# Optimization experiments

Hardware: AMD Instinct MI355X
Metric: run time of the kernel (lower is better)

The kernel has to match this reference:

```python
import jax, jax.numpy as jnp
import numpy as np

NDIM = 1024
NHEAD = 16
HEAD_DIM = NDIM // NHEAD


def setup_inputs() -> dict:
    key = jax.random.key(0)
    ks = jax.random.split(key, 12)
    B, L, C = 2, 2048, NDIM
    s = 0.02
    return {
        "q": jax.random.normal(ks[0], (B, L, C), jnp.float32),
        "k": jax.random.normal(ks[1], (B, L, C), jnp.float32),
        "v": jax.random.normal(ks[2], (B, L, C), jnp.float32),
        "Wq": jax.random.normal(ks[3], (C, C), jnp.float32) * s,
        "bq": jax.random.normal(ks[4], (C,), jnp.float32) * s,
        "Wk": jax.random.normal(ks[5], (C, C), jnp.float32) * s,
        "bk": jax.random.normal(ks[6], (C,), jnp.float32) * s,
        "Wv": jax.random.normal(ks[7], (C, C), jnp.float32) * s,
        "bv": jax.random.normal(ks[8], (C,), jnp.float32) * s,
        "Wo": jax.random.normal(ks[9], (C, C), jnp.float32) * s,
        "bo": jax.random.normal(ks[10], (C,), jnp.float32) * s,
    }


def reference(q, k, v, Wq, bq, Wk, bk, Wv, bv, Wo, bo):
    B, Lq, C = q.shape
    H, D = NHEAD, HEAD_DIM
    # projections, then split heads: (B, H, L, D)
    qh = (q @ Wq + bq).reshape(B, Lq, H, D).transpose(0, 2, 1, 3)
    kh = (k @ Wk + bk).reshape(B, k.shape[1], H, D).transpose(0, 2, 1, 3)
    vh = (v @ Wv + bv).reshape(B, v.shape[1], H, D).transpose(0, 2, 1, 3)
    scale = 1.0 / jnp.sqrt(jnp.asarray(D, qh.dtype))
    att = jnp.einsum("bhqd,bhkd->bhqk", qh, kh) * scale  # (B,H,Lq,Lk)
    att = jax.nn.softmax(att, axis=-1)  # dropout p=0.0 -> identity
    y = jnp.einsum("bhqk,bhkd->bhqd", att, vh)
    y = y.transpose(0, 2, 1, 3).reshape(B, Lq, C)
    return y @ Wo + bo
```

## Files before the change

kernel.cpp:

```cpp
#include <hip/hip_runtime.h>
#include <math.h>

#define BATCH 2
#define SEQ   2048
#define CDIM  1024
#define NHEAD 16
#define HDIM  64
#define TOKS  (BATCH * SEQ)

typedef __bf16 bf16x8 __attribute__((ext_vector_type(8)));
typedef __bf16 bf16x2 __attribute__((ext_vector_type(2)));
typedef float  f32x4  __attribute__((ext_vector_type(4)));
typedef float  f32x16 __attribute__((ext_vector_type(16)));

#define MFMA16(a, b, c) __builtin_amdgcn_mfma_f32_16x16x32_bf16(a, b, c, 0, 0, 0)
#define MFMA32(a, b, c) __builtin_amdgcn_mfma_f32_32x32x16_bf16(a, b, c, 0, 0, 0)

#define QSCALE 0.1803368801111204f

__device__ __forceinline__ void gload_lds16(const __bf16* g, __bf16* l) {
    __builtin_amdgcn_global_load_lds(
        (const __attribute__((address_space(1))) unsigned int*)g,
        (__attribute__((address_space(3))) unsigned int*)l, 16, 0, 0);
}

__global__ __launch_bounds__(256) void prep_kernel(
    const float* __restrict__ q, const float* __restrict__ k, const float* __restrict__ v,
    __bf16* __restrict__ qo, __bf16* __restrict__ ko, __bf16* __restrict__ vo,
    const float* __restrict__ W0, const float* __restrict__ W1,
    const float* __restrict__ W2, const float* __restrict__ W3,
    __bf16* __restrict__ T0, __bf16* __restrict__ T1,
    __bf16* __restrict__ T2, __bf16* __restrict__ T3)
{
    __shared__ __bf16 Ts[64][72];
    const int bx = blockIdx.x;
    const int tid = threadIdx.x;

    if (bx < 6144) {
        const int t = bx >> 11;
        const size_t i = ((size_t)(bx & 2047) * 256 + tid) * 8;
        const float* s = t == 0 ? q : (t == 1 ? k : v);
        __bf16* d = t == 0 ? qo : (t == 1 ? ko : vo);
        const float4 x = *(const float4*)&s[i];
        const float4 y = *(const float4*)&s[i + 4];
        bf16x8 o;
        o[0] = (__bf16)x.x; o[1] = (__bf16)x.y; o[2] = (__bf16)x.z; o[3] = (__bf16)x.w;
        o[4] = (__bf16)y.x; o[5] = (__bf16)y.y; o[6] = (__bf16)y.z; o[7] = (__bf16)y.w;
        *(bf16x8*)&d[i] = o;
        return;
    }

    const int t  = bx - 6144;
    const int z  = t >> 8;
    const int ry = (t & 255) >> 4;
    const int rx = t & 15;
    const float* W = z == 0 ? W0 : z == 1 ? W1 : z == 2 ? W2 : W3;
    __bf16* T = z == 0 ? T0 : z == 1 ? T1 : z == 2 ? T2 : T3;
    const int rb = ry * 64, cb = rx * 64;
    const int r = tid >> 4;
    const int c4 = (tid & 15) * 4;
#pragma unroll
    for (int p = 0; p < 4; p++) {
        const int rr = p * 16 + r;
        const float4 w4 = *(const float4*)&W[(size_t)(rb + rr) * CDIM + cb + c4];
        Ts[c4 + 0][rr] = (__bf16)w4.x;
        Ts[c4 + 1][rr] = (__bf16)w4.y;
        Ts[c4 + 2][rr] = (__bf16)w4.z;
        Ts[c4 + 3][rr] = (__bf16)w4.w;
    }
    __syncthreads();
    const int n = tid >> 2;
    const int k16 = (tid & 3) * 16;
    *(bf16x8*)&T[(size_t)(cb + n) * CDIM + rb + k16]     = *(const bf16x8*)&Ts[n][k16];
    *(bf16x8*)&T[(size_t)(cb + n) * CDIM + rb + k16 + 8] = *(const bf16x8*)&Ts[n][k16 + 8];
}

__global__ __launch_bounds__(512, 6) void qkv_gemm_kernel(
    const __bf16* __restrict__ qb, const __bf16* __restrict__ kb,
    const __bf16* __restrict__ vb,
    const __bf16* __restrict__ Wqt, const __bf16* __restrict__ Wkt,
    const __bf16* __restrict__ Wvt,
    const float* __restrict__ bq, const float* __restrict__ bk,
    const float* __restrict__ bv,
    __bf16* __restrict__ Qh, __bf16* __restrict__ Kh, __bf16* __restrict__ Vht)
{
    __shared__ __bf16 As[128 * 32];
    __shared__ __bf16 Bs[128 * 32];

    const int lin = blockIdx.x + (blockIdx.y << 3) + (blockIdx.z << 8);
    const int nl  = (lin & 7) * 96 + (lin >> 3);
    const int bx  = nl & 7;
    const int by  = (nl >> 3) & 31;
    const int z   = nl >> 8;

    const __bf16* A    = z == 0 ? qb : z == 1 ? kb : Wvt;
    const __bf16* Bt   = z == 0 ? Wqt : z == 1 ? Wkt : vb;
    const float*  bias = z == 0 ? bq : z == 1 ? bk : bv;

    const int tid  = threadIdx.x;
    const int w    = tid >> 6;
    const int lane = tid & 63;
    const int quad = lane >> 4;
    const int c    = lane & 15;
    const int wm   = w >> 1;
    const int wn   = w & 1;
    const int rowBase = (z == 2 ? bx : by) * 128;
    const int colBase = (z == 2 ? by : bx) * 128;

    const int sr = lane >> 2;
    const int sk = (lane & 3) * 8;

    f32x4 acc[2][4];
#pragma unroll
    for (int i = 0; i < 2; i++)
#pragma unroll
        for (int j = 0; j < 4; j++) acc[i][j] = (f32x4){0, 0, 0, 0};

    const __bf16* srcA = A  + (size_t)(rowBase + w * 16 + sr) * CDIM + sk;
    const __bf16* srcB = Bt + (size_t)(colBase + w * 16 + sr) * CDIM + sk;
    __bf16* dstA = &As[w * 16 * 32];
    __bf16* dstB = &Bs[w * 16 * 32];

    for (int k0 = 0; k0 < CDIM; k0 += 32) {
        gload_lds16(srcA + k0, dstA);
        gload_lds16(srcB + k0, dstB);
        __syncthreads();

        bf16x8 af[2], bf[4];
#pragma unroll
        for (int i = 0; i < 2; i++)
            af[i] = *(const bf16x8*)&As[(wm * 32 + i * 16 + c) * 32 + quad * 8];
#pragma unroll
        for (int i = 0; i < 4; i++)
            bf[i] = *(const bf16x8*)&Bs[(wn * 64 + i * 16 + c) * 32 + quad * 8];
#pragma unroll
        for (int mi = 0; mi < 2; mi++)
#pragma unroll
            for (int ni = 0; ni < 4; ni++)
                acc[mi][ni] = MFMA16(af[mi], bf[ni], acc[mi][ni]);
        __syncthreads();
    }

#pragma unroll
    for (int mi = 0; mi < 2; mi++) {
#pragma unroll
        for (int ni = 0; ni < 4; ni++) {
            const int col = colBase + wn * 64 + ni * 16 + c;
#pragma unroll
            for (int r = 0; r < 4; r++) {
                const int row = rowBase + wm * 32 + mi * 16 + quad * 4 + r;
                const float val = acc[mi][ni][r];
                if (z == 2) {
                    Vht[(size_t)row * TOKS + col] = (__bf16)(val + bias[row]);
                } else {
                    const int b = row >> 11, l = row & 2047;
                    const int h = col >> 6,  d = col & 63;
                    const float s = (z == 0) ? QSCALE : 1.0f;
                    __bf16* outp = (z == 0) ? Qh : Kh;
                    outp[((((size_t)b * NHEAD + h) * SEQ) + l) * HDIM + d] =
                        (__bf16)((val + bias[col]) * s);
                }
            }
        }
    }
}

__global__ __launch_bounds__(512, 4) void out_gemm_kernel(
    const __bf16* __restrict__ A, const __bf16* __restrict__ Bt,
    const float* __restrict__ bias, float* __restrict__ out)
{
    __shared__ __bf16 As[128 * 32];
    __shared__ __bf16 Bs[64 * 32];

    const int lin = blockIdx.x + (blockIdx.y << 4);
    const int nl  = (lin & 7) * 64 + (lin >> 3);
    const int bx  = nl & 15;
    const int by  = nl >> 4;

    const int tid  = threadIdx.x;
    const int w    = tid >> 6;
    const int lane = tid & 63;
    const int quad = lane >> 4;
    const int c    = lane & 15;
    const int wm   = w >> 1;
    const int wn   = w & 1;
    const int rowBase = by * 128;
    const int colBase = bx * 64;
    const int sr = lane >> 2;
    const int sk = (lane & 3) * 8;

    f32x4 acc[2][2];
#pragma unroll
    for (int i = 0; i < 2; i++)
#pragma unroll
        for (int j = 0; j < 2; j++) acc[i][j] = (f32x4){0, 0, 0, 0};

    const __bf16* srcA = A + (size_t)(rowBase + w * 16 + sr) * CDIM + sk;
    const __bf16* srcB = Bt + (size_t)(colBase + (w & 3) * 16 + sr) * CDIM + sk;
    __bf16* dstA = &As[w * 16 * 32];
    __bf16* dstB = &Bs[(w & 3) * 16 * 32];

    for (int k0 = 0; k0 < CDIM; k0 += 32) {
        gload_lds16(srcA + k0, dstA);
        if (w < 4) gload_lds16(srcB + k0, dstB);
        __syncthreads();

        bf16x8 af[2], bf[2];
#pragma unroll
        for (int i = 0; i < 2; i++)
            af[i] = *(const bf16x8*)&As[(wm * 32 + i * 16 + c) * 32 + quad * 8];
#pragma unroll
        for (int i = 0; i < 2; i++)
            bf[i] = *(const bf16x8*)&Bs[(wn * 32 + i * 16 + c) * 32 + quad * 8];
#pragma unroll
        for (int mi = 0; mi < 2; mi++)
#pragma unroll
            for (int ni = 0; ni < 2; ni++)
                acc[mi][ni] = MFMA16(af[mi], bf[ni], acc[mi][ni]);
        __syncthreads();
    }

#pragma unroll
    for (int mi = 0; mi < 2; mi++) {
#pragma unroll
        for (int ni = 0; ni < 2; ni++) {
            const int col = colBase + wn * 32 + ni * 16 + c;
#pragma unroll
            for (int r = 0; r < 4; r++) {
                const int row = rowBase + wm * 32 + mi * 16 + quad * 4 + r;
                out[(size_t)row * CDIM + col] = acc[mi][ni][r] + bias[col];
            }
        }
    }
}

__global__ __launch_bounds__(256, 2) void attn_v10_kernel(
    const __bf16* __restrict__ Qh, const __bf16* __restrict__ Kh,
    const __bf16* __restrict__ Vht, __bf16* __restrict__ Y)
{
    __shared__ __align__(16) __bf16 Ks[2][128][64];
    __shared__ __align__(16) __bf16 Vt[2][64][128];

    const int tid  = threadIdx.x;
    const int w    = tid >> 6;
    const int lane = tid & 63;
    const int l31  = lane & 31;
    const int hi   = lane >> 5;
    const int swz  = l31 & 7;
    const int bh   = blockIdx.x;
    const int b    = bh >> 4;
    const int h    = bh & 15;
    const int qbase = blockIdx.y * 128 + w * 32;

    const __bf16* Qg = Qh + (size_t)bh * SEQ * HDIM;
    const __bf16* Kg = Kh + (size_t)bh * SEQ * HDIM;
    const __bf16* Vg = Vht + (size_t)(h * HDIM) * TOKS + (size_t)b * SEQ;

    bf16x8 qf[4];
#pragma unroll
    for (int ks = 0; ks < 4; ks++)
        qf[ks] = *(const bf16x8*)&Qg[(size_t)(qbase + l31) * HDIM + ks * 16 + hi * 8];

    bf16x8 ones;
#pragma unroll
    for (int j = 0; j < 8; j++) ones[j] = (__bf16)1.0f;

    f32x16 O0, O1, LA;
#pragma unroll
    for (int j = 0; j < 16; j++) { O0[j] = 0.0f; O1[j] = 0.0f; LA[j] = 0.0f; }

    const int kr8 = lane >> 3, kc = lane & 7;
    const int vr4 = lane >> 4, vc = lane & 15;

#define STAGE(T, bb)                                                          \
    {                                                                         \
        _Pragma("unroll")                                                     \
        for (int jj = 0; jj < 4; jj++) {                                      \
            const int j = w * 4 + jj;                                         \
            gload_lds16(Kg + (size_t)((T) + 8 * j + kr8) * HDIM               \
                           + ((kc ^ kr8) * 8),                                \
                        &Ks[bb][8 * j][0]);                                   \
            gload_lds16(Vg + (size_t)(4 * j + vr4) * TOKS + (T)               \
                           + ((vc ^ ((4 * j + vr4) & 7)) * 8),                \
                        &Vt[bb][4 * j][0]);                                   \
        }                                                                     \
    }

    STAGE(0, 0);
    __syncthreads();

    int buf = 0;
    for (int t0 = 0; t0 < SEQ; t0 += 128) {
        const int tn = t0 + 128;
        if (tn < SEQ) {
            if (buf == 0) STAGE(tn, 1) else STAGE(tn, 0)
        }

#pragma unroll
        for (int kt = 0; kt < 4; kt++) {
            f32x16 st0, st1;
#pragma unroll
            for (int j = 0; j < 16; j++) { st0[j] = 0.0f; st1[j] = 0.0f; }
            const bf16x8 kf0 = *(const bf16x8*)&Ks[buf][kt * 32 + l31][((0 + hi) ^ swz) * 8];
            const bf16x8 kf1 = *(const bf16x8*)&Ks[buf][kt * 32 + l31][((2 + hi) ^ swz) * 8];
            const bf16x8 kf2 = *(const bf16x8*)&Ks[buf][kt * 32 + l31][((4 + hi) ^ swz) * 8];
            const bf16x8 kf3 = *(const bf16x8*)&Ks[buf][kt * 32 + l31][((6 + hi) ^ swz) * 8];
            st0 = MFMA32(kf0, qf[0], st0);
            st1 = MFMA32(kf1, qf[1], st1);
            st0 = MFMA32(kf2, qf[2], st0);
            st1 = MFMA32(kf3, qf[3], st1);

            float p[16];
#pragma unroll
            for (int j = 0; j < 16; j++)
                p[j] = __builtin_amdgcn_exp2f(st0[j] + st1[j]);

#pragma unroll
            for (int kl = 0; kl < 2; kl++) {
                const int r0 = kl * 8;
                union { bf16x2 v; unsigned int u; } pa, pb, pc, pd;
                pa.v[0] = (__bf16)p[r0 + 0]; pa.v[1] = (__bf16)p[r0 + 1];
                pb.v[0] = (__bf16)p[r0 + 2]; pb.v[1] = (__bf16)p[r0 + 3];
                pc.v[0] = (__bf16)p[r0 + 4]; pc.v[1] = (__bf16)p[r0 + 5];
                pd.v[0] = (__bf16)p[r0 + 6]; pd.v[1] = (__bf16)p[r0 + 7];
                asm volatile("v_permlane32_swap_b32 %0, %1"
                             : "+v"(pa.u), "+v"(pc.u));
                asm volatile("v_permlane32_swap_b32 %0, %1"
                             : "+v"(pb.u), "+v"(pd.u));
                union { unsigned int u[4]; bf16x8 v; } af;
                af.u[0] = pa.u; af.u[1] = pb.u; af.u[2] = pc.u; af.u[3] = pd.u;
                const int cc = kt * 4 + kl * 2 + hi;
                const bf16x8 vf0 = *(const bf16x8*)&Vt[buf][l31][(cc ^ swz) * 8];
                const bf16x8 vf1 = *(const bf16x8*)&Vt[buf][32 + l31][(cc ^ swz) * 8];
                __builtin_amdgcn_s_setprio(1);
                LA = MFMA32(af.v, ones, LA);
                O0 = MFMA32(af.v, vf0, O0);
                O1 = MFMA32(af.v, vf1, O1);
                __builtin_amdgcn_s_setprio(0);
            }
        }

        __syncthreads();
        buf ^= 1;
    }
#undef STAGE

    __bf16* Yb = Y + (size_t)b * SEQ * CDIM;
#pragma unroll
    for (int reg = 0; reg < 16; reg++) {
        const int qrow  = (reg & 3) + 8 * (reg >> 2) + 4 * hi;
        const float iq  = 1.0f / LA[reg];
        __bf16* yp = Yb + (size_t)(qbase + qrow) * CDIM + h * HDIM + l31;
        yp[0]  = (__bf16)(O0[reg] * iq);
        yp[32] = (__bf16)(O1[reg] * iq);
    }
}


extern "C" void kernel_launch(void* const* d_in, const int* in_sizes, int n_in,
                              void* d_out, int out_size, void* d_ws, size_t ws_size,
                              hipStream_t stream)
{
    const float* q  = (const float*)d_in[0];
    const float* k  = (const float*)d_in[1];
    const float* v  = (const float*)d_in[2];
    const float* Wq = (const float*)d_in[3];
    const float* bq = (const float*)d_in[4];
    const float* Wk = (const float*)d_in[5];
    const float* bk = (const float*)d_in[6];
    const float* Wv = (const float*)d_in[7];
    const float* bv = (const float*)d_in[8];
    const float* Wo = (const float*)d_in[9];
    const float* bo = (const float*)d_in[10];
    float* out = (float*)d_out;

    const size_t MAT = (size_t)TOKS * CDIM;
    const size_t WN  = (size_t)CDIM * CDIM;

    __bf16* p   = (__bf16*)d_ws;
    __bf16* qb  = p; p += MAT;
    __bf16* kb  = p; p += MAT;
    __bf16* vb  = p; p += MAT;
    __bf16* Wqt = p; p += WN;
    __bf16* Wkt = p; p += WN;
    __bf16* Wvt = p; p += WN;
    __bf16* Wot = p; p += WN;
    __bf16* Qh  = p; p += MAT;
    __bf16* Kh  = p; p += MAT;
    __bf16* Vht = p; p += MAT;
    __bf16* Yb  = qb;

    prep_kernel<<<dim3(7168), dim3(256), 0, stream>>>(
        q, k, v, qb, kb, vb, Wq, Wk, Wv, Wo, Wqt, Wkt, Wvt, Wot);

    qkv_gemm_kernel<<<dim3(8, 32, 3), dim3(512), 0, stream>>>(
        qb, kb, vb, Wqt, Wkt, Wvt, bq, bk, bv, Qh, Kh, Vht);

    attn_v10_kernel<<<dim3(BATCH * NHEAD, SEQ / 128), dim3(256), 0, stream>>>(Qh, Kh, Vht, Yb);

    out_gemm_kernel<<<dim3(16, 32), dim3(512), 0, stream>>>(Yb, Wot, bo, out);
}
```

Measured before the change: 218.7 us.

## Split attention key range across two wave groups and reduce partials via LDS

The attention kernel now launches 512 threads per block. The two halves of the waves each process half of the key sequence (1024 keys) for the same 128 query rows. Partial O and row-sum accumulators are combined through LDS scratch at the end. This doubles the waves per block and halves each wave's serial loop length, aiming for more latency hiding and occupancy. The cost is an extra reduction step and a barrier. There is no running max, so like the code before it relies on unnormalized exp2 staying in range.

```diff
diff --git a/kernel.cpp b/kernel.cpp
--- a/kernel.cpp
+++ b/kernel.cpp
@@ -234,15 +234,17 @@
     }
 }
 
-__global__ __launch_bounds__(256, 2) void attn_v10_kernel(
+__global__ __launch_bounds__(512, 4) void attn_v11_kernel(
     const __bf16* __restrict__ Qh, const __bf16* __restrict__ Kh,
     const __bf16* __restrict__ Vht, __bf16* __restrict__ Y)
 {
-    __shared__ __align__(16) __bf16 Ks[2][128][64];
-    __shared__ __align__(16) __bf16 Vt[2][64][128];
+    __shared__ __align__(16) __bf16 Ks[2][2][64][64];
+    __shared__ __align__(16) __bf16 Vt[2][2][64][64];
 
     const int tid  = threadIdx.x;
     const int w    = tid >> 6;
+    const int wq   = w & 3;
+    const int half = w >> 2;
     const int lane = tid & 63;
     const int l31  = lane & 31;
     const int hi   = lane >> 5;
@@ -250,7 +252,7 @@
     const int bh   = blockIdx.x;
     const int b    = bh >> 4;
     const int h    = bh & 15;
-    const int qbase = blockIdx.y * 128 + w * 32;
+    const int qbase = blockIdx.y * 128 + wq * 32;
 
     const __bf16* Qg = Qh + (size_t)bh * SEQ * HDIM;
     const __bf16* Kg = Kh + (size_t)bh * SEQ * HDIM;
@@ -270,19 +272,22 @@
     for (int j = 0; j < 16; j++) { O0[j] = 0.0f; O1[j] = 0.0f; LA[j] = 0.0f; }
 
     const int kr8 = lane >> 3, kc = lane & 7;
-    const int vr4 = lane >> 4, vc = lane & 15;
 
 #define STAGE(T, bb)                                                          \
     {                                                                         \
         _Pragma("unroll")                                                     \
         for (int jj = 0; jj < 4; jj++) {                                      \
-            const int j = w * 4 + jj;                                         \
-            gload_lds16(Kg + (size_t)((T) + 8 * j + kr8) * HDIM               \
-                           + ((kc ^ kr8) * 8),                                \
-                        &Ks[bb][8 * j][0]);                                   \
-            gload_lds16(Vg + (size_t)(4 * j + vr4) * TOKS + (T)               \
-                           + ((vc ^ ((4 * j + vr4) & 7)) * 8),                \
-                        &Vt[bb][4 * j][0]);                                   \
+            const int cch = w * 4 + jj;                                       \
+            const int s  = (cch >> 3) & 1;                                    \
+            const int j  = cch & 7;                                           \
+            if (cch < 16)                                                     \
+                gload_lds16(Kg + (size_t)(s * 1024 + (T) + 8 * j + kr8) * HDIM \
+                               + ((kc ^ kr8) * 8),                            \
+                            &Ks[bb][s][8 * j][0]);                            \
+            else                                                              \
+                gload_lds16(Vg + (size_t)(8 * j + kr8) * TOKS                 \
+                               + s * 1024 + (T) + ((kc ^ kr8) * 8),           \
+                            &Vt[bb][s][8 * j][0]);                            \
         }                                                                     \
     }
 
@@ -290,30 +295,30 @@
     __syncthreads();
 
     int buf = 0;
-    for (int t0 = 0; t0 < SEQ; t0 += 128) {
-        const int tn = t0 + 128;
-        if (tn < SEQ) {
+    for (int t0 = 0; t0 < 1024; t0 += 64) {
+        const int tn = t0 + 64;
+        if (tn < 1024) {
             if (buf == 0) STAGE(tn, 1) else STAGE(tn, 0)
         }
 
 #pragma unroll
-        for (int kt = 0; kt < 4; kt++) {
-            f32x16 st0, st1;
-#pragma unroll
-            for (int j = 0; j < 16; j++) { st0[j] = 0.0f; st1[j] = 0.0f; }
-            const bf16x8 kf0 = *(const bf16x8*)&Ks[buf][kt * 32 + l31][((0 + hi) ^ swz) * 8];
-            const bf16x8 kf1 = *(const bf16x8*)&Ks[buf][kt * 32 + l31][((2 + hi) ^ swz) * 8];
-            const bf16x8 kf2 = *(const bf16x8*)&Ks[buf][kt * 32 + l31][((4 + hi) ^ swz) * 8];
-            const bf16x8 kf3 = *(const bf16x8*)&Ks[buf][kt * 32 + l31][((6 + hi) ^ swz) * 8];
-            st0 = MFMA32(kf0, qf[0], st0);
-            st1 = MFMA32(kf1, qf[1], st1);
-            st0 = MFMA32(kf2, qf[2], st0);
-            st1 = MFMA32(kf3, qf[3], st1);
+        for (int kt = 0; kt < 2; kt++) {
+            f32x16 st;
+#pragma unroll
+            for (int j = 0; j < 16; j++) st[j] = 0.0f;
+            const bf16x8 kf0 = *(const bf16x8*)&Ks[buf][half][kt * 32 + l31][((0 + hi) ^ swz) * 8];
+            const bf16x8 kf1 = *(const bf16x8*)&Ks[buf][half][kt * 32 + l31][((2 + hi) ^ swz) * 8];
+            const bf16x8 kf2 = *(const bf16x8*)&Ks[buf][half][kt * 32 + l31][((4 + hi) ^ swz) * 8];
+            const bf16x8 kf3 = *(const bf16x8*)&Ks[buf][half][kt * 32 + l31][((6 + hi) ^ swz) * 8];
+            st = MFMA32(kf0, qf[0], st);
+            st = MFMA32(kf1, qf[1], st);
+            st = MFMA32(kf2, qf[2], st);
+            st = MFMA32(kf3, qf[3], st);
 
             float p[16];
 #pragma unroll
             for (int j = 0; j < 16; j++)
-                p[j] = __builtin_amdgcn_exp2f(st0[j] + st1[j]);
+                p[j] = __builtin_amdgcn_exp2f(st[j]);
 
 #pragma unroll
             for (int kl = 0; kl < 2; kl++) {
@@ -330,8 +335,8 @@
                 union { unsigned int u[4]; bf16x8 v; } af;
                 af.u[0] = pa.u; af.u[1] = pb.u; af.u[2] = pc.u; af.u[3] = pd.u;
                 const int cc = kt * 4 + kl * 2 + hi;
-                const bf16x8 vf0 = *(const bf16x8*)&Vt[buf][l31][(cc ^ swz) * 8];
-                const bf16x8 vf1 = *(const bf16x8*)&Vt[buf][32 + l31][(cc ^ swz) * 8];
+                const bf16x8 vf0 = *(const bf16x8*)&Vt[buf][half][l31][(cc ^ swz) * 8];
+                const bf16x8 vf1 = *(const bf16x8*)&Vt[buf][half][32 + l31][(cc ^ swz) * 8];
                 __builtin_amdgcn_s_setprio(1);
                 LA = MFMA32(af.v, ones, LA);
                 O0 = MFMA32(af.v, vf0, O0);
@@ -345,14 +350,28 @@
     }
 #undef STAGE
 
-    __bf16* Yb = Y + (size_t)b * SEQ * CDIM;
-#pragma unroll
-    for (int reg = 0; reg < 16; reg++) {
-        const int qrow  = (reg & 3) + 8 * (reg >> 2) + 4 * hi;
-        const float iq  = 1.0f / LA[reg];
-        __bf16* yp = Yb + (size_t)(qbase + qrow) * CDIM + h * HDIM + l31;
-        yp[0]  = (__bf16)(O0[reg] * iq);
-        yp[32] = (__bf16)(O1[reg] * iq);
+    float* scr  = (float*)&Ks[0][0][0][0];
+    float* scr2 = (float*)&Vt[0][0][0][0];
+    if (half == 1) {
+        *(f32x16*)&scr [(wq * 64 + lane) * 16]        = O0;
+        *(f32x16*)&scr [4096 + (wq * 64 + lane) * 16] = O1;
+        *(f32x16*)&scr2[(wq * 64 + lane) * 16]        = LA;
+    }
+    __syncthreads();
+    if (half == 0) {
+        O0 += *(const f32x16*)&scr [(wq * 64 + lane) * 16];
+        O1 += *(const f32x16*)&scr [4096 + (wq * 64 + lane) * 16];
+        LA += *(const f32x16*)&scr2[(wq * 64 + lane) * 16];
+
+        __bf16* Yb = Y + (size_t)b * SEQ * CDIM;
+#pragma unroll
+        for (int reg = 0; reg < 16; reg++) {
+            const int qrow  = (reg & 3) + 8 * (reg >> 2) + 4 * hi;
+            const float iq  = 1.0f / LA[reg];
+            __bf16* yp = Yb + (size_t)(qbase + qrow) * CDIM + h * HDIM + l31;
+            yp[0]  = (__bf16)(O0[reg] * iq);
+            yp[32] = (__bf16)(O1[reg] * iq);
+        }
     }
 }
 
@@ -396,7 +415,7 @@
     qkv_gemm_kernel<<<dim3(8, 32, 3), dim3(512), 0, stream>>>(
         qb, kb, vb, Wqt, Wkt, Wvt, bq, bk, bv, Qh, Kh, Vht);
 
-    attn_v10_kernel<<<dim3(BATCH * NHEAD, SEQ / 128), dim3(256), 0, stream>>>(Qh, Kh, Vht, Yb);
+    attn_v11_kernel<<<dim3(BATCH * NHEAD, SEQ / 128), dim3(512), 0, stream>>>(Qh, Kh, Vht, Yb);
 
     out_gemm_kernel<<<dim3(16, 32), dim3(512), 0, stream>>>(Yb, Wot, bo, out);
 }
```

Measured after the change: 217.2 us. Within noise of the previous version (-0.7%).

## Split attention KV range across wave pairs, each wave handling 64 query rows

Applied to the files above, without the earlier changes.

Each wave now computes 64 query rows (two 32-row tiles) instead of 32, so every K and V fragment read from LDS feeds twice as many MFMAs. The four waves split into two pairs that each handle half of the key sequence, and the partial O and row-sum accumulators are merged through LDS at the end. The LDS layout changes to padded 520-element blocks with XOR swizzle to avoid bank conflicts. The cost is more accumulator registers per wave, which may pressure occupancy at launch bounds of 2, plus an extra merge pass and barrier.

```diff
diff --git a/kernel.cpp b/kernel.cpp
--- a/kernel.cpp
+++ b/kernel.cpp
@@ -234,108 +234,134 @@
     }
 }
 
-__global__ __launch_bounds__(256, 2) void attn_v10_kernel(
+__global__ __launch_bounds__(256, 2) void attn_v12_kernel(
     const __bf16* __restrict__ Qh, const __bf16* __restrict__ Kh,
     const __bf16* __restrict__ Vht, __bf16* __restrict__ Y)
 {
-    __shared__ __align__(16) __bf16 Ks[2][128][64];
-    __shared__ __align__(16) __bf16 Vt[2][64][128];
+    __shared__ __align__(16) __bf16 lds[2][2][2][8 * 520];
 
     const int tid  = threadIdx.x;
     const int w    = tid >> 6;
+    const int wq   = w & 1;
+    const int kh   = w >> 1;
     const int lane = tid & 63;
     const int l31  = lane & 31;
     const int hi   = lane >> 5;
-    const int swz  = l31 & 7;
+    const int rr8  = l31 & 7;
+    const int cb   = (l31 >> 3) * 520 + rr8 * 64;
     const int bh   = blockIdx.x;
     const int b    = bh >> 4;
     const int h    = bh & 15;
-    const int qbase = blockIdx.y * 128 + w * 32;
-
-    const __bf16* Qg = Qh + (size_t)bh * SEQ * HDIM;
-    const __bf16* Kg = Kh + (size_t)bh * SEQ * HDIM;
-    const __bf16* Vg = Vht + (size_t)(h * HDIM) * TOKS + (size_t)b * SEQ;
-
-    bf16x8 qf[4];
-#pragma unroll
-    for (int ks = 0; ks < 4; ks++)
-        qf[ks] = *(const bf16x8*)&Qg[(size_t)(qbase + l31) * HDIM + ks * 16 + hi * 8];
+    const int qbase = blockIdx.y * 128 + wq * 64;
+
+    const __bf16* Qg  = Qh + (size_t)bh * SEQ * HDIM;
+    const __bf16* KgB = Kh + (size_t)bh * SEQ * HDIM;
+    const __bf16* VgB = Vht + (size_t)(h * HDIM) * TOKS + (size_t)b * SEQ;
+
+    bf16x8 qf0[4], qf1[4];
+#pragma unroll
+    for (int ks = 0; ks < 4; ks++) {
+        qf0[ks] = *(const bf16x8*)&Qg[(size_t)(qbase + l31) * HDIM + ks * 16 + hi * 8];
+        qf1[ks] = *(const bf16x8*)&Qg[(size_t)(qbase + 32 + l31) * HDIM + ks * 16 + hi * 8];
+    }
 
     bf16x8 ones;
 #pragma unroll
     for (int j = 0; j < 8; j++) ones[j] = (__bf16)1.0f;
 
-    f32x16 O0, O1, LA;
-#pragma unroll
-    for (int j = 0; j < 16; j++) { O0[j] = 0.0f; O1[j] = 0.0f; LA[j] = 0.0f; }
-
+    f32x16 O00, O01, O10, O11, LA0, LA1;
+#pragma unroll
+    for (int j = 0; j < 16; j++) {
+        O00[j] = 0.0f; O01[j] = 0.0f; O10[j] = 0.0f; O11[j] = 0.0f;
+        LA0[j] = 0.0f; LA1[j] = 0.0f;
+    }
+
+    const int sidx = w & 1;
+    const int iskv = w >> 1;
     const int kr8 = lane >> 3, kc = lane & 7;
-    const int vr4 = lane >> 4, vc = lane & 15;
 
 #define STAGE(T, bb)                                                          \
     {                                                                         \
         _Pragma("unroll")                                                     \
-        for (int jj = 0; jj < 4; jj++) {                                      \
-            const int j = w * 4 + jj;                                         \
-            gload_lds16(Kg + (size_t)((T) + 8 * j + kr8) * HDIM               \
-                           + ((kc ^ kr8) * 8),                                \
-                        &Ks[bb][8 * j][0]);                                   \
-            gload_lds16(Vg + (size_t)(4 * j + vr4) * TOKS + (T)               \
-                           + ((vc ^ ((4 * j + vr4) & 7)) * 8),                \
-                        &Vt[bb][4 * j][0]);                                   \
+        for (int jj = 0; jj < 8; jj++) {                                      \
+            if (iskv == 0)                                                    \
+                gload_lds16(KgB + (size_t)(sidx * 1024 + (T) + 8 * jj + kr8) * HDIM \
+                                + ((kc ^ kr8) * 8),                           \
+                            &lds[bb][sidx][0][jj * 520]);                     \
+            else                                                              \
+                gload_lds16(VgB + (size_t)(8 * jj + kr8) * TOKS               \
+                                + sidx * 1024 + (T) + ((kc ^ kr8) * 8),       \
+                            &lds[bb][sidx][1][jj * 520]);                     \
         }                                                                     \
+    }
+
+#define PACK_AF(P, KL, AF)                                                    \
+    {                                                                         \
+        const int r0 = (KL) * 8;                                              \
+        union { bf16x2 v; unsigned int u; } pa, pb, pc, pd;                   \
+        pa.v[0] = (__bf16)P[r0 + 0]; pa.v[1] = (__bf16)P[r0 + 1];             \
+        pb.v[0] = (__bf16)P[r0 + 2]; pb.v[1] = (__bf16)P[r0 + 3];             \
+        pc.v[0] = (__bf16)P[r0 + 4]; pc.v[1] = (__bf16)P[r0 + 5];             \
+        pd.v[0] = (__bf16)P[r0 + 6]; pd.v[1] = (__bf16)P[r0 + 7];             \
+        asm volatile("v_permlane32_swap_b32 %0, %1" : "+v"(pa.u), "+v"(pc.u)); \
+        asm volatile("v_permlane32_swap_b32 %0, %1" : "+v"(pb.u), "+v"(pd.u)); \
+        AF.u[0] = pa.u; AF.u[1] = pb.u; AF.u[2] = pc.u; AF.u[3] = pd.u;       \
     }
 
     STAGE(0, 0);
     __syncthreads();
 
     int buf = 0;
-    for (int t0 = 0; t0 < SEQ; t0 += 128) {
-        const int tn = t0 + 128;
-        if (tn < SEQ) {
+    for (int t0 = 0; t0 < 1024; t0 += 64) {
+        const int tn = t0 + 64;
+        if (tn < 1024) {
             if (buf == 0) STAGE(tn, 1) else STAGE(tn, 0)
         }
 
-#pragma unroll
-        for (int kt = 0; kt < 4; kt++) {
-            f32x16 st0, st1;
-#pragma unroll
-            for (int j = 0; j < 16; j++) { st0[j] = 0.0f; st1[j] = 0.0f; }
-            const bf16x8 kf0 = *(const bf16x8*)&Ks[buf][kt * 32 + l31][((0 + hi) ^ swz) * 8];
-            const bf16x8 kf1 = *(const bf16x8*)&Ks[buf][kt * 32 + l31][((2 + hi) ^ swz) * 8];
-            const bf16x8 kf2 = *(const bf16x8*)&Ks[buf][kt * 32 + l31][((4 + hi) ^ swz) * 8];
-            const bf16x8 kf3 = *(const bf16x8*)&Ks[buf][kt * 32 + l31][((6 + hi) ^ swz) * 8];
-            st0 = MFMA32(kf0, qf[0], st0);
-            st1 = MFMA32(kf1, qf[1], st1);
-            st0 = MFMA32(kf2, qf[2], st0);
-            st1 = MFMA32(kf3, qf[3], st1);
-
-            float p[16];
-#pragma unroll
-            for (int j = 0; j < 16; j++)
-                p[j] = __builtin_amdgcn_exp2f(st0[j] + st1[j]);
+        const __bf16* ldsK = &lds[buf][kh][0][0];
+        const __bf16* ldsV = &lds[buf][kh][1][0];
+
+#pragma unroll
+        for (int kt = 0; kt < 2; kt++) {
+            const bf16x8 kf0 = *(const bf16x8*)&ldsK[kt * 2080 + cb + (((0 + hi) ^ rr8) * 8)];
+            const bf16x8 kf1 = *(const bf16x8*)&ldsK[kt * 2080 + cb + (((2 + hi) ^ rr8) * 8)];
+            const bf16x8 kf2 = *(const bf16x8*)&ldsK[kt * 2080 + cb + (((4 + hi) ^ rr8) * 8)];
+            const bf16x8 kf3 = *(const bf16x8*)&ldsK[kt * 2080 + cb + (((6 + hi) ^ rr8) * 8)];
+
+            f32x16 s0, s1;
+#pragma unroll
+            for (int j = 0; j < 16; j++) { s0[j] = 0.0f; s1[j] = 0.0f; }
+            s0 = MFMA32(kf0, qf0[0], s0);
+            s1 = MFMA32(kf0, qf1[0], s1);
+            s0 = MFMA32(kf1, qf0[1], s0);
+            s1 = MFMA32(kf1, qf1[1], s1);
+            s0 = MFMA32(kf2, qf0[2], s0);
+            s1 = MFMA32(kf2, qf1[2], s1);
+            s0 = MFMA32(kf3, qf0[3], s0);
+            s1 = MFMA32(kf3, qf1[3], s1);
+
+            float p0[16], p1[16];
+#pragma unroll
+            for (int j = 0; j < 16; j++) {
+                p0[j] = __builtin_amdgcn_exp2f(s0[j]);
+                p1[j] = __builtin_amdgcn_exp2f(s1[j]);
+            }
 
 #pragma unroll
             for (int kl = 0; kl < 2; kl++) {
-                const int r0 = kl * 8;
-                union { bf16x2 v; unsigned int u; } pa, pb, pc, pd;
-                pa.v[0] = (__bf16)p[r0 + 0]; pa.v[1] = (__bf16)p[r0 + 1];
-                pb.v[0] = (__bf16)p[r0 + 2]; pb.v[1] = (__bf16)p[r0 + 3];
-                pc.v[0] = (__bf16)p[r0 + 4]; pc.v[1] = (__bf16)p[r0 + 5];
-                pd.v[0] = (__bf16)p[r0 + 6]; pd.v[1] = (__bf16)p[r0 + 7];
-                asm volatile("v_permlane32_swap_b32 %0, %1"
-                             : "+v"(pa.u), "+v"(pc.u));
-                asm volatile("v_permlane32_swap_b32 %0, %1"
-                             : "+v"(pb.u), "+v"(pd.u));
-                union { unsigned int u[4]; bf16x8 v; } af;
-                af.u[0] = pa.u; af.u[1] = pb.u; af.u[2] = pc.u; af.u[3] = pd.u;
-                const int cc = kt * 4 + kl * 2 + hi;
-                const bf16x8 vf0 = *(const bf16x8*)&Vt[buf][l31][(cc ^ swz) * 8];
-                const bf16x8 vf1 = *(const bf16x8*)&Vt[buf][32 + l31][(cc ^ swz) * 8];
+                union AFU { unsigned int u[4]; bf16x8 v; } af0, af1;
+                PACK_AF(p0, kl, af0);
+                PACK_AF(p1, kl, af1);
+                const int sv = (((kt * 4 + kl * 2 + hi) ^ rr8) * 8);
+                const bf16x8 vf0 = *(const bf16x8*)&ldsV[cb + sv];
+                const bf16x8 vf1 = *(const bf16x8*)&ldsV[2080 + cb + sv];
                 __builtin_amdgcn_s_setprio(1);
-                LA = MFMA32(af.v, ones, LA);
-                O0 = MFMA32(af.v, vf0, O0);
-                O1 = MFMA32(af.v, vf1, O1);
+                LA0 = MFMA32(af0.v, ones, LA0);
+                O00 = MFMA32(af0.v, vf0, O00);
+                O01 = MFMA32(af0.v, vf1, O01);
+                LA1 = MFMA32(af1.v, ones, LA1);
+                O10 = MFMA32(af1.v, vf0, O10);
+                O11 = MFMA32(af1.v, vf1, O11);
                 __builtin_amdgcn_s_setprio(0);
             }
         }
@@ -345,15 +371,48 @@
     }
 #undef STAGE
 
-    __bf16* Yb = Y + (size_t)b * SEQ * CDIM;
-#pragma unroll
-    for (int reg = 0; reg < 16; reg++) {
-        const int qrow  = (reg & 3) + 8 * (reg >> 2) + 4 * hi;
-        const float iq  = 1.0f / LA[reg];
-        __bf16* yp = Yb + (size_t)(qbase + qrow) * CDIM + h * HDIM + l31;
-        yp[0]  = (__bf16)(O0[reg] * iq);
-        yp[32] = (__bf16)(O1[reg] * iq);
-    }
+    float* scr = (float*)&lds[0][0][0][0];
+    const int wl = wq * 64 + lane;
+
+#define SPILL(OP, OPI)                                                        \
+    { union { f32x16 v; f32x4 q[4]; } tt; tt.v = OP;                          \
+      _Pragma("unroll")                                                       \
+      for (int part = 0; part < 4; part++)                                    \
+          *(f32x4*)&scr[(((OPI) * 4 + part) * 128 + wl) * 4] = tt.q[part]; }
+
+#define MERGE(OP, OPI)                                                        \
+    { union { f32x16 v; f32x4 q[4]; } tt; tt.v = OP;                          \
+      _Pragma("unroll")                                                       \
+      for (int part = 0; part < 4; part++)                                    \
+          tt.q[part] += *(const f32x4*)&scr[(((OPI) * 4 + part) * 128 + wl) * 4]; \
+      OP = tt.v; }
+
+    if (kh == 1) {
+        SPILL(O00, 0); SPILL(O01, 1); SPILL(O10, 2);
+        SPILL(O11, 3); SPILL(LA0, 4); SPILL(LA1, 5);
+    }
+    __syncthreads();
+    if (kh == 0) {
+        MERGE(O00, 0); MERGE(O01, 1); MERGE(O10, 2);
+        MERGE(O11, 3); MERGE(LA0, 4); MERGE(LA1, 5);
+
+        __bf16* Yb = Y + (size_t)b * SEQ * CDIM;
+#pragma unroll
+        for (int reg = 0; reg < 16; reg++) {
+            const int qrow = (reg & 3) + 8 * (reg >> 2) + 4 * hi;
+            const float i0 = 1.0f / LA0[reg];
+            const float i1 = 1.0f / LA1[reg];
+            __bf16* yp0 = Yb + (size_t)(qbase + qrow) * CDIM + h * HDIM + l31;
+            __bf16* yp1 = Yb + (size_t)(qbase + 32 + qrow) * CDIM + h * HDIM + l31;
+            yp0[0]  = (__bf16)(O00[reg] * i0);
+            yp0[32] = (__bf16)(O01[reg] * i0);
+            yp1[0]  = (__bf16)(O10[reg] * i1);
+            yp1[32] = (__bf16)(O11[reg] * i1);
+        }
+    }
+#undef SPILL
+#undef MERGE
+#undef PACK_AF
 }
 
 
@@ -396,7 +455,7 @@
     qkv_gemm_kernel<<<dim3(8, 32, 3), dim3(512), 0, stream>>>(
         qb, kb, vb, Wqt, Wkt, Wvt, bq, bk, bv, Qh, Kh, Vht);
 
-    attn_v10_kernel<<<dim3(BATCH * NHEAD, SEQ / 128), dim3(256), 0, stream>>>(Qh, Kh, Vht, Yb);
+    attn_v12_kernel<<<dim3(BATCH * NHEAD, SEQ / 128), dim3(256), 0, stream>>>(Qh, Kh, Vht, Yb);
 
     out_gemm_kernel<<<dim3(16, 32), dim3(512), 0, stream>>>(Yb, Wot, bo, out);
 }
```

Result: no change. 221.4 us (+1.2%).
